# Kernel optimization log

Measured on AMD Instinct MI355X. Metric: run time of the kernel, lower is better.

The kernel has to match this reference:

```python
import jax, jax.numpy as jnp
import numpy as np

D_MODEL = 1024
HEADS = 16
D_K = D_MODEL // HEADS
B, S = 2, 2048
NEG = -1000000000.0

def setup_inputs() -> dict:
    key = jax.random.key(0)
    ks = jax.random.split(key, 11)
    sc = 1.0 / np.sqrt(D_MODEL)
    inp = {
        'q': jax.random.normal(ks[0], (B, S, D_MODEL), jnp.float32),
        'k': jax.random.normal(ks[1], (B, S, D_MODEL), jnp.float32),
        'v': jax.random.normal(ks[2], (B, S, D_MODEL), jnp.float32),
        'mask': jnp.tril(jnp.ones((S, S), jnp.int32))[None, None],  # causal [1,1,S,S]
        'wq_w': jax.random.normal(ks[3], (D_MODEL, D_MODEL), jnp.float32) * sc,
        'wq_b': jax.random.normal(ks[4], (D_MODEL,), jnp.float32) * 0.02,
        'wk_w': jax.random.normal(ks[5], (D_MODEL, D_MODEL), jnp.float32) * sc,
        'wk_b': jax.random.normal(ks[6], (D_MODEL,), jnp.float32) * 0.02,
        'wv_w': jax.random.normal(ks[7], (D_MODEL, D_MODEL), jnp.float32) * sc,
        'wv_b': jax.random.normal(ks[8], (D_MODEL,), jnp.float32) * 0.02,
        'wo_w': jax.random.normal(ks[9], (D_MODEL, D_MODEL), jnp.float32) * sc,
        'wo_b': jax.random.normal(ks[10], (D_MODEL,), jnp.float32) * 0.02,
    }
    return inp

def reference(q, k, v, mask, wq_w, wq_b, wk_w, wk_b, wv_w, wv_b, wo_w, wo_b):
    b, s, _ = q.shape
    # projections (torch Linear: x @ W^T + b)
    Q = (q @ wq_w.T + wq_b).reshape(b, s, HEADS, D_K).transpose(0, 2, 1, 3)  # [B,H,S,Dk]
    K = (k @ wk_w.T + wk_b).reshape(b, s, HEADS, D_K).transpose(0, 2, 1, 3)
    V = (v @ wv_w.T + wv_b).reshape(b, s, HEADS, D_K).transpose(0, 2, 1, 3)
    scores = jnp.einsum('bhqd,bhkd->bhqk', Q, K) / jnp.sqrt(jnp.float32(D_K))
    scores = jnp.where(mask == 0, NEG, scores)
    p = jax.nn.softmax(scores, axis=-1)  # dropout=0.0 -> identity
    x = jnp.einsum('bhqk,bhkd->bhqd', p, V)
    x = x.transpose(0, 2, 1, 3).reshape(b, s, D_MODEL)
    return x @ wo_w.T + wo_b
```

## Files before the change

kernel.cpp:

```cpp
#include <hip/hip_runtime.h>

typedef unsigned short u16;
typedef __attribute__((ext_vector_type(8))) short bf16x8;
typedef __attribute__((ext_vector_type(4))) float f32x4;

#define SEQ 2048
#define DMODEL 1024

__device__ __forceinline__ u16 f2bf(float f) {
    union { float f; unsigned u; } x; x.f = f;
    unsigned r = x.u + 0x7fffu + ((x.u >> 16) & 1u);
    return (u16)(r >> 16);
}

__device__ __forceinline__ u16 f2bf_trunc(float f) {
    union { float f; unsigned u; } x; x.f = f;
    return (u16)(x.u >> 16);
}

__device__ __forceinline__ float bf2f(u16 v) {
    union { unsigned u; float f; } x; x.u = ((unsigned)v) << 16;
    return x.f;
}

__device__ __forceinline__ f32x4 mfma16(bf16x8 a, bf16x8 b, f32x4 c) {
    return __builtin_amdgcn_mfma_f32_16x16x32_bf16(a, b, c, 0, 0, 0);
}

__device__ __forceinline__ void gld16(const u16* g, u16* l) {
    __builtin_amdgcn_global_load_lds(
        (__attribute__((address_space(1))) const void*)g,
        (__attribute__((address_space(3))) void*)l, 16, 0, 0);
}

struct CvtArgs {
    const float* src[7];
    u16* dst[7];
    int n4[7];
};

__global__ __launch_bounds__(256) void cvt_kernel(CvtArgs a) {
    const int id = blockIdx.y;
    const int i = blockIdx.x * 256 + threadIdx.x;
    if (i >= a.n4[id]) return;
    float4 f = ((const float4*)a.src[id])[i];
    ushort4 u;
    u.x = f2bf(f.x); u.y = f2bf(f.y); u.z = f2bf(f.z); u.w = f2bf(f.w);
    ((ushort4*)a.dst[id])[i] = u;
}


__global__ __launch_bounds__(512, 2) void gemm_qkv(
    const u16* __restrict__ Xq, const u16* __restrict__ Xk, const u16* __restrict__ Xv,
    const u16* __restrict__ Wq, const u16* __restrict__ Wk, const u16* __restrict__ Wv,
    const float* __restrict__ bq, const float* __restrict__ bk, const float* __restrict__ bv,
    u16* __restrict__ Qb, u16* __restrict__ Kb, u16* __restrict__ Vb)
{
    __shared__ u16 Abuf[2][256 * 64];
    __shared__ u16 Bbuf[2][256 * 64];

    const int bid = blockIdx.x;
    const int G = (bid & 7) * 24 + (bid >> 3);
    const int z = G >> 6;
    const int rem = G & 63;
    const int bm = (rem >> 2) * 256;
    const int bn = (rem & 3) * 256;

    const u16* X = (z == 0) ? Xq : (z == 1) ? Xk : Xv;
    const u16* W = (z == 0) ? Wq : (z == 1) ? Wk : Wv;
    const float* bias = (z == 0) ? bq : (z == 1) ? bk : bv;

    const int tid = threadIdx.x;
    const int lane = tid & 63, w = tid >> 6;
    const int wr = w >> 2, wc = w & 3;
    const int r = lane & 15, qd = lane >> 4;

    const int srow = lane >> 3;
    const int scol = ((lane & 7) ^ srow) * 8;
    const u16* Xs = X + (size_t)(bm + w * 32 + srow) * 1024 + scol;
    const u16* Ws = W + (size_t)(bn + w * 32 + srow) * 1024 + scol;

    const int rxor = (r & 7) << 4;
    const int rowA = (wr * 128 + r) * 128;
    const int rowB = (wc * 64 + r) * 128;
    const int ko0 = (qd * 16) ^ rxor;
    const int ko1 = (64 + qd * 16) ^ rxor;

    f32x4 acc[8][4];
    #pragma unroll
    for (int i = 0; i < 8; ++i)
        #pragma unroll
        for (int j = 0; j < 4; ++j)
            acc[i][j] = (f32x4){0.f, 0.f, 0.f, 0.f};

    auto stage = [&](int t) {
        const int d = t & 1;
        const u16* xa = Xs + t * 64;
        const u16* wb = Ws + t * 64;
        u16* Al = &Abuf[d][w * 2048];
        u16* Bl = &Bbuf[d][w * 2048];
        #pragma unroll
        for (int q = 0; q < 4; ++q) {
            gld16(xa + (size_t)q * 8192, Al + q * 512);
            gld16(wb + (size_t)q * 8192, Bl + q * 512);
        }
    };

    stage(0);
    stage(1);
    asm volatile("s_waitcnt vmcnt(8)" ::: "memory");
    __builtin_amdgcn_sched_barrier(0);
    __builtin_amdgcn_s_barrier();

    for (int t = 0; t < 16; ++t) {
        const u16* Ab = Abuf[t & 1];
        const u16* Bb = Bbuf[t & 1];
        #pragma unroll
        for (int kc = 0; kc < 2; ++kc) {
            const int ko = kc ? ko1 : ko0;
            bf16x8 aF[8], bF[4];
            #pragma unroll
            for (int m = 0; m < 8; ++m)
                aF[m] = *(const bf16x8*)((const char*)Ab + rowA + m * 2048 + ko);
            #pragma unroll
            for (int n = 0; n < 4; ++n)
                bF[n] = *(const bf16x8*)((const char*)Bb + rowB + n * 2048 + ko);
            __builtin_amdgcn_s_setprio(1);
            #pragma unroll
            for (int m = 0; m < 8; ++m)
                #pragma unroll
                for (int n = 0; n < 4; ++n)
                    acc[m][n] = mfma16(aF[m], bF[n], acc[m][n]);
            __builtin_amdgcn_s_setprio(0);
        }
        if (t == 15) break;
        asm volatile("s_waitcnt lgkmcnt(0)" ::: "memory");
        __builtin_amdgcn_sched_barrier(0);
        __builtin_amdgcn_s_barrier();
        if (t < 14) {
            stage(t + 2);
            asm volatile("s_waitcnt vmcnt(8)" ::: "memory");
        } else {
            asm volatile("s_waitcnt vmcnt(0)" ::: "memory");
        }
        __builtin_amdgcn_sched_barrier(0);
        __builtin_amdgcn_s_barrier();
        __builtin_amdgcn_sched_barrier(0);
    }

    const float scale = (z == 0) ? 0.125f : 1.0f;
    #pragma unroll
    for (int j = 0; j < 4; ++j) {
        const int n = bn + wc * 64 + j * 16 + r;
        const float bvl = bias[n];
        const int h = n >> 6, d = n & 63;
        #pragma unroll
        for (int i = 0; i < 8; ++i) {
            const int m0 = bm + wr * 128 + i * 16 + qd * 4;
            const int b_ = m0 >> 11, s0 = m0 & 2047;
            if (z == 0) {
                #pragma unroll
                for (int reg = 0; reg < 4; ++reg)
                    Qb[(size_t)(m0 + reg) * 1024 + n] = f2bf((acc[i][j][reg] + bvl) * scale);
            } else if (z == 1) {
                #pragma unroll
                for (int reg = 0; reg < 4; ++reg)
                    Kb[((size_t)(b_ * 16 + h) * SEQ + s0 + reg) * 64 + d] =
                        f2bf(acc[i][j][reg] + bvl);
            } else {
                ushort4 u;
                u.x = f2bf(acc[i][j][0] + bvl);
                u.y = f2bf(acc[i][j][1] + bvl);
                u.z = f2bf(acc[i][j][2] + bvl);
                u.w = f2bf(acc[i][j][3] + bvl);
                *(ushort4*)(Vb + ((size_t)(b_ * 16 + h) * 64 + d) * SEQ + s0) = u;
            }
        }
    }
}

__global__ __launch_bounds__(128, 3) void attn_kernel(
    const u16* __restrict__ Qb, const u16* __restrict__ Kb,
    const u16* __restrict__ Vb, u16* __restrict__ Op, float* __restrict__ Lp)
{
    __shared__ u16 Kst[2][4096];
    __shared__ u16 Vst[2][4096];
    __shared__ u16 Pst[2][16 * 72];

    const int bid = blockIdx.x;
    const int xcd = bid & 7;
    const int i2 = bid >> 3;
    const int bh = xcd + 8 * (i2 & 3);
    const int rest = i2 >> 2;
    const int g = 31 - (rest >> 1);
    const int half = rest & 1;
    const int b_ = bh >> 4, h = bh & 15;

    const int h0 = (g + 1) >> 1;
    const int j0 = half ? h0 : 0;
    const int j1 = half ? (g + 1) : h0;

    const int tid = threadIdx.x;
    const int lane = tid & 63, w = tid >> 6;
    const int r = lane & 15, qd = lane >> 4;

    const u16* Kh = Kb + (size_t)bh * SEQ * 64;
    const u16* Vh = Vb + (size_t)bh * 64 * SEQ;
    u16* Pw = Pst[w];

    bf16x8 aQ[2][2];
    #pragma unroll
    for (int i = 0; i < 2; ++i) {
        const size_t qoff =
            (size_t)(b_ * SEQ + g * 64 + w * 32 + i * 16 + r) * DMODEL + h * 64;
        aQ[i][0] = *(const bf16x8*)(Qb + qoff + qd * 8);
        aQ[i][1] = *(const bf16x8*)(Qb + qoff + 32 + qd * 8);
    }

    bf16x8 ones;
    #pragma unroll
    for (int e = 0; e < 8; ++e) ones[e] = (short)0x3F80;

    f32x4 o[2][4];
    f32x4 l[2];
    #pragma unroll
    for (int i = 0; i < 2; ++i) {
        l[i] = (f32x4){0.f, 0.f, 0.f, 0.f};
        #pragma unroll
        for (int db = 0; db < 4; ++db) o[i][db] = (f32x4){0.f, 0.f, 0.f, 0.f};
    }

    auto stage = [&](int j, int buf) {
        if (w == 0) {
            const u16* Kt = Kh + (size_t)j * 64 * 64;
            #pragma unroll
            for (int s = 0; s < 8; ++s)
                gld16(Kt + ((s >> 1) * 16 + r) * 64 + (s & 1) * 32 + qd * 8,
                      &Kst[buf][s * 512]);
        } else {
            const u16* Vt = Vh + j * 64;
            #pragma unroll
            for (int s = 0; s < 8; ++s)
                gld16(Vt + (size_t)((s >> 1) * 16 + r) * SEQ + (s & 1) * 32 + qd * 8,
                      &Vst[buf][s * 512]);
        }
    };

    if (j0 < j1) stage(j0, j0 & 1);

    for (int j = j0; j < j1; ++j) {
        const int cur = j & 1;
        __syncthreads();
        if (j + 1 < j1) stage(j + 1, 1 - cur);

        bf16x8 kf[4][2], vf[4][2];
        #pragma unroll
        for (int nb = 0; nb < 4; ++nb) {
            kf[nb][0] = *(const bf16x8*)(&Kst[cur][(nb * 2 + 0) * 512 + lane * 8]);
            kf[nb][1] = *(const bf16x8*)(&Kst[cur][(nb * 2 + 1) * 512 + lane * 8]);
        }
        #pragma unroll
        for (int db = 0; db < 4; ++db) {
            vf[db][0] = *(const bf16x8*)(&Vst[cur][(db * 2 + 0) * 512 + lane * 8]);
            vf[db][1] = *(const bf16x8*)(&Vst[cur][(db * 2 + 1) * 512 + lane * 8]);
        }

        #pragma unroll
        for (int i = 0; i < 2; ++i) {
            f32x4 sc[4];
            #pragma unroll
            for (int nb = 0; nb < 4; ++nb) {
                f32x4 s = (f32x4){0.f, 0.f, 0.f, 0.f};
                s = mfma16(kf[nb][0], aQ[i][0], s);
                s = mfma16(kf[nb][1], aQ[i][1], s);
                sc[nb] = s;
            }

            if (j == g) {
                const int rowr = w * 32 + i * 16 + r;
                #pragma unroll
                for (int nb = 0; nb < 4; ++nb)
                    #pragma unroll
                    for (int reg = 0; reg < 4; ++reg)
                        if (nb * 16 + qd * 4 + reg > rowr) sc[nb][reg] = -1e30f;
            }

            #pragma unroll
            for (int nb = 0; nb < 4; ++nb)
                #pragma unroll
                for (int reg = 0; reg < 4; ++reg)
                    sc[nb][reg] = exp2f(fmaf(sc[nb][reg], 1.4426950408889634f,
                                             -23.083120654223414f));

            #pragma unroll
            for (int nb = 0; nb < 4; ++nb) {
                ushort4 pk;
                pk.x = f2bf_trunc(sc[nb][0]);
                pk.y = f2bf_trunc(sc[nb][1]);
                pk.z = f2bf_trunc(sc[nb][2]);
                pk.w = f2bf_trunc(sc[nb][3]);
                *(ushort4*)(Pw + r * 72 + nb * 16 + qd * 4) = pk;
            }

            const bf16x8 aP0 = *(const bf16x8*)(Pw + r * 72 + qd * 8);
            const bf16x8 aP1 = *(const bf16x8*)(Pw + r * 72 + 32 + qd * 8);

            l[i] = mfma16(aP0, ones, l[i]);
            l[i] = mfma16(aP1, ones, l[i]);

            #pragma unroll
            for (int db = 0; db < 4; ++db) {
                o[i][db] = mfma16(aP0, vf[db][0], o[i][db]);
                o[i][db] = mfma16(aP1, vf[db][1], o[i][db]);
            }
        }
    }

    u16* Oh = Op + ((size_t)(half * 1024 + bh * 32 + g) * 4096);
    float* Lh = Lp + (size_t)(half * 1024 + bh * 32 + g) * 64;
    #pragma unroll
    for (int i = 0; i < 2; ++i) {
        #pragma unroll
        for (int db = 0; db < 4; ++db)
            #pragma unroll
            for (int reg = 0; reg < 4; ++reg)
                Oh[(w * 32 + i * 16 + qd * 4 + reg) * 64 + db * 16 + r] =
                    f2bf(o[i][db][reg]);
        if (r == 0) {
            #pragma unroll
            for (int reg = 0; reg < 4; ++reg)
                Lh[w * 32 + i * 16 + qd * 4 + reg] = l[i][reg];
        }
    }
}

__global__ __launch_bounds__(256) void attn_norm(
    const u16* __restrict__ Op, const float* __restrict__ Lp,
    u16* __restrict__ AO)
{
    const int idx = blockIdx.x * 256 + threadIdx.x;
    const int col8 = idx & 127;
    const int row = idx >> 7;
    const int h = col8 >> 3;
    const int b_ = row >> 11, s = row & 2047;
    const int g = s >> 6, r64 = s & 63;
    const int bh = b_ * 16 + h;

    const size_t pa = ((size_t)(bh * 32 + g) * 4096) + r64 * 64 + (col8 & 7) * 8;
    const size_t pb = pa + (size_t)1024 * 4096;
    const float la = Lp[(bh * 32 + g) * 64 + r64];
    const float lb = Lp[(1024 + bh * 32 + g) * 64 + r64];
    const float inv = 1.0f / (la + lb);

    const bf16x8 a = *(const bf16x8*)(Op + pa);
    const bf16x8 b = *(const bf16x8*)(Op + pb);
    bf16x8 o;
    #pragma unroll
    for (int e = 0; e < 8; ++e)
        o[e] = (short)f2bf((bf2f((u16)a[e]) + bf2f((u16)b[e])) * inv);
    *(bf16x8*)(AO + (size_t)row * 1024 + col8 * 8) = o;
}

__global__ __launch_bounds__(512, 2) void gemm_out(
    const u16* __restrict__ AO, const u16* __restrict__ W,
    const float* __restrict__ bias, float* __restrict__ out)
{
    __shared__ u16 Abuf[2][256 * 64];
    __shared__ u16 Bbuf[2][256 * 64];

    const int bid = blockIdx.x;
    const int G = (bid & 7) * 8 + (bid >> 3);
    const int bm = (G >> 2) * 256;
    const int bn = (G & 3) * 256;

    const int tid = threadIdx.x;
    const int lane = tid & 63, w = tid >> 6;
    const int wr = w >> 2, wc = w & 3;
    const int r = lane & 15, qd = lane >> 4;

    const int srow = lane >> 3;
    const int scol = ((lane & 7) ^ srow) * 8;
    const u16* Xs = AO + (size_t)(bm + w * 32 + srow) * 1024 + scol;
    const u16* Ws = W + (size_t)(bn + w * 32 + srow) * 1024 + scol;

    const int rxor = (r & 7) << 4;
    const int rowA = (wr * 128 + r) * 128;
    const int rowB = (wc * 64 + r) * 128;
    const int ko0 = (qd * 16) ^ rxor;
    const int ko1 = (64 + qd * 16) ^ rxor;

    f32x4 acc[8][4];
    #pragma unroll
    for (int i = 0; i < 8; ++i)
        #pragma unroll
        for (int j = 0; j < 4; ++j)
            acc[i][j] = (f32x4){0.f, 0.f, 0.f, 0.f};

    auto stage = [&](int t) {
        const int d = t & 1;
        const u16* xa = Xs + t * 64;
        const u16* wb = Ws + t * 64;
        u16* Al = &Abuf[d][w * 2048];
        u16* Bl = &Bbuf[d][w * 2048];
        #pragma unroll
        for (int q = 0; q < 4; ++q) {
            gld16(xa + (size_t)q * 8192, Al + q * 512);
            gld16(wb + (size_t)q * 8192, Bl + q * 512);
        }
    };

    stage(0);
    stage(1);
    asm volatile("s_waitcnt vmcnt(8)" ::: "memory");
    __builtin_amdgcn_sched_barrier(0);
    __builtin_amdgcn_s_barrier();

    for (int t = 0; t < 16; ++t) {
        const u16* Ab = Abuf[t & 1];
        const u16* Bb = Bbuf[t & 1];
        #pragma unroll
        for (int kc = 0; kc < 2; ++kc) {
            const int ko = kc ? ko1 : ko0;
            bf16x8 aF[8], bF[4];
            #pragma unroll
            for (int m = 0; m < 8; ++m)
                aF[m] = *(const bf16x8*)((const char*)Ab + rowA + m * 2048 + ko);
            #pragma unroll
            for (int n = 0; n < 4; ++n)
                bF[n] = *(const bf16x8*)((const char*)Bb + rowB + n * 2048 + ko);
            __builtin_amdgcn_s_setprio(1);
            #pragma unroll
            for (int m = 0; m < 8; ++m)
                #pragma unroll
                for (int n = 0; n < 4; ++n)
                    acc[m][n] = mfma16(aF[m], bF[n], acc[m][n]);
            __builtin_amdgcn_s_setprio(0);
        }
        if (t == 15) break;
        asm volatile("s_waitcnt lgkmcnt(0)" ::: "memory");
        __builtin_amdgcn_sched_barrier(0);
        __builtin_amdgcn_s_barrier();
        if (t < 14) {
            stage(t + 2);
            asm volatile("s_waitcnt vmcnt(8)" ::: "memory");
        } else {
            asm volatile("s_waitcnt vmcnt(0)" ::: "memory");
        }
        __builtin_amdgcn_sched_barrier(0);
        __builtin_amdgcn_s_barrier();
        __builtin_amdgcn_sched_barrier(0);
    }

    #pragma unroll
    for (int j = 0; j < 4; ++j) {
        const int n = bn + wc * 64 + j * 16 + r;
        const float bvl = bias[n];
        #pragma unroll
        for (int i = 0; i < 8; ++i) {
            const int m0 = bm + wr * 128 + i * 16 + qd * 4;
            #pragma unroll
            for (int reg = 0; reg < 4; ++reg)
                out[(size_t)(m0 + reg) * 1024 + n] = acc[i][j][reg] + bvl;
        }
    }
}

extern "C" void kernel_launch(void* const* d_in, const int* in_sizes, int n_in,
                              void* d_out, int out_size, void* d_ws, size_t ws_size,
                              hipStream_t stream) {
    const float* q  = (const float*)d_in[0];
    const float* k  = (const float*)d_in[1];
    const float* v  = (const float*)d_in[2];
    const float* wq = (const float*)d_in[4];
    const float* bq = (const float*)d_in[5];
    const float* wk = (const float*)d_in[6];
    const float* bk = (const float*)d_in[7];
    const float* wv = (const float*)d_in[8];
    const float* bv = (const float*)d_in[9];
    const float* wo = (const float*)d_in[10];
    const float* bo = (const float*)d_in[11];
    float* out = (float*)d_out;

    u16* ws = (u16*)d_ws;
    u16* Xq = ws;
    u16* Xk = Xq + (size_t)4194304;
    u16* Xv = Xk + (size_t)4194304;
    u16* Wq = Xv + (size_t)4194304;
    u16* Wk = Wq + (size_t)1048576;
    u16* Wv = Wk + (size_t)1048576;
    u16* Wo = Wv + (size_t)1048576;
    u16* Qb = Wo + (size_t)1048576;
    u16* Kb = Qb + (size_t)4194304;
    u16* Vb = Kb + (size_t)4194304;
    u16* AO = Vb + (size_t)4194304;

    u16* Op = ws;
    float* Lp = (float*)(ws + (size_t)8388608);

    CvtArgs ca;
    ca.src[0] = q;  ca.dst[0] = Xq; ca.n4[0] = 1048576;
    ca.src[1] = k;  ca.dst[1] = Xk; ca.n4[1] = 1048576;
    ca.src[2] = v;  ca.dst[2] = Xv; ca.n4[2] = 1048576;
    ca.src[3] = wq; ca.dst[3] = Wq; ca.n4[3] = 262144;
    ca.src[4] = wk; ca.dst[4] = Wk; ca.n4[4] = 262144;
    ca.src[5] = wv; ca.dst[5] = Wv; ca.n4[5] = 262144;
    ca.src[6] = wo; ca.dst[6] = Wo; ca.n4[6] = 262144;

    cvt_kernel<<<dim3(4096, 7), 256, 0, stream>>>(ca);
    gemm_qkv<<<dim3(192), 512, 0, stream>>>(Xq, Xk, Xv, Wq, Wk, Wv,
                                            bq, bk, bv, Qb, Kb, Vb);
    attn_kernel<<<dim3(2048), 128, 0, stream>>>(Qb, Kb, Vb, Op, Lp);
    attn_norm<<<dim3(2048), 256, 0, stream>>>(Op, Lp, AO);
    gemm_out<<<dim3(256 / 4), 512, 0, stream>>>(AO, Wo, bo, out);
}
```

Baseline: 258.3 us.

## Split causal attention KV range into thirds with four waves per block

The attention kernel now splits each query tile's causal KV range three ways instead of two, and uses four waves of 16 query rows each instead of two waves of 32 rows. The grid grows from 2048 to 3072 blocks of 256 threads. The normalisation kernel merges three partial outputs and three partial sums, and the Lp workspace offset moves to make room for the third partial. The aim is more parallelism and smaller per-thread register state for better occupancy, at the cost of one more partial write and read and less K/V reuse per block.

```diff
diff --git a/kernel.cpp b/kernel.cpp
--- a/kernel.cpp
+++ b/kernel.cpp
@@ -179,26 +179,27 @@
     }
 }
 
-__global__ __launch_bounds__(128, 3) void attn_kernel(
+__global__ __launch_bounds__(256, 3) void attn_kernel(
     const u16* __restrict__ Qb, const u16* __restrict__ Kb,
     const u16* __restrict__ Vb, u16* __restrict__ Op, float* __restrict__ Lp)
 {
     __shared__ u16 Kst[2][4096];
     __shared__ u16 Vst[2][4096];
-    __shared__ u16 Pst[2][16 * 72];
+    __shared__ u16 Pst[4][16 * 72];
 
     const int bid = blockIdx.x;
     const int xcd = bid & 7;
     const int i2 = bid >> 3;
     const int bh = xcd + 8 * (i2 & 3);
     const int rest = i2 >> 2;
-    const int g = 31 - (rest >> 1);
-    const int half = rest & 1;
+    const int gidx = rest / 3;
+    const int third = rest - gidx * 3;
+    const int g = 31 - gidx;
     const int b_ = bh >> 4, h = bh & 15;
 
-    const int h0 = (g + 1) >> 1;
-    const int j0 = half ? h0 : 0;
-    const int j1 = half ? (g + 1) : h0;
+    const int n = g + 1;
+    const int j0 = (n * third) / 3;
+    const int j1 = (n * (third + 1)) / 3;
 
     const int tid = threadIdx.x;
     const int lane = tid & 63, w = tid >> 6;
@@ -208,41 +209,40 @@
     const u16* Vh = Vb + (size_t)bh * 64 * SEQ;
     u16* Pw = Pst[w];
 
-    bf16x8 aQ[2][2];
-    #pragma unroll
-    for (int i = 0; i < 2; ++i) {
+    bf16x8 aQ[2];
+    {
         const size_t qoff =
-            (size_t)(b_ * SEQ + g * 64 + w * 32 + i * 16 + r) * DMODEL + h * 64;
-        aQ[i][0] = *(const bf16x8*)(Qb + qoff + qd * 8);
-        aQ[i][1] = *(const bf16x8*)(Qb + qoff + 32 + qd * 8);
+            (size_t)(b_ * SEQ + g * 64 + w * 16 + r) * DMODEL + h * 64;
+        aQ[0] = *(const bf16x8*)(Qb + qoff + qd * 8);
+        aQ[1] = *(const bf16x8*)(Qb + qoff + 32 + qd * 8);
     }
 
     bf16x8 ones;
     #pragma unroll
     for (int e = 0; e < 8; ++e) ones[e] = (short)0x3F80;
 
-    f32x4 o[2][4];
-    f32x4 l[2];
-    #pragma unroll
-    for (int i = 0; i < 2; ++i) {
-        l[i] = (f32x4){0.f, 0.f, 0.f, 0.f};
-        #pragma unroll
-        for (int db = 0; db < 4; ++db) o[i][db] = (f32x4){0.f, 0.f, 0.f, 0.f};
-    }
+    f32x4 o[4];
+    f32x4 l = (f32x4){0.f, 0.f, 0.f, 0.f};
+    #pragma unroll
+    for (int db = 0; db < 4; ++db) o[db] = (f32x4){0.f, 0.f, 0.f, 0.f};
 
     auto stage = [&](int j, int buf) {
-        if (w == 0) {
+        if (w < 2) {
             const u16* Kt = Kh + (size_t)j * 64 * 64;
             #pragma unroll
-            for (int s = 0; s < 8; ++s)
-                gld16(Kt + ((s >> 1) * 16 + r) * 64 + (s & 1) * 32 + qd * 8,
-                      &Kst[buf][s * 512]);
+            for (int s = 0; s < 4; ++s) {
+                const int ss = w * 4 + s;
+                gld16(Kt + ((ss >> 1) * 16 + r) * 64 + (ss & 1) * 32 + qd * 8,
+                      &Kst[buf][ss * 512]);
+            }
         } else {
             const u16* Vt = Vh + j * 64;
             #pragma unroll
-            for (int s = 0; s < 8; ++s)
-                gld16(Vt + (size_t)((s >> 1) * 16 + r) * SEQ + (s & 1) * 32 + qd * 8,
-                      &Vst[buf][s * 512]);
+            for (int s = 0; s < 4; ++s) {
+                const int ss = (w - 2) * 4 + s;
+                gld16(Vt + (size_t)((ss >> 1) * 16 + r) * SEQ + (ss & 1) * 32 + qd * 8,
+                      &Vst[buf][ss * 512]);
+            }
         }
     };
 
@@ -265,72 +265,65 @@
             vf[db][1] = *(const bf16x8*)(&Vst[cur][(db * 2 + 1) * 512 + lane * 8]);
         }
 
-        #pragma unroll
-        for (int i = 0; i < 2; ++i) {
-            f32x4 sc[4];
-            #pragma unroll
-            for (int nb = 0; nb < 4; ++nb) {
-                f32x4 s = (f32x4){0.f, 0.f, 0.f, 0.f};
-                s = mfma16(kf[nb][0], aQ[i][0], s);
-                s = mfma16(kf[nb][1], aQ[i][1], s);
-                sc[nb] = s;
-            }
-
-            if (j == g) {
-                const int rowr = w * 32 + i * 16 + r;
-                #pragma unroll
-                for (int nb = 0; nb < 4; ++nb)
-                    #pragma unroll
-                    for (int reg = 0; reg < 4; ++reg)
-                        if (nb * 16 + qd * 4 + reg > rowr) sc[nb][reg] = -1e30f;
-            }
-
+        f32x4 sc[4];
+        #pragma unroll
+        for (int nb = 0; nb < 4; ++nb) {
+            f32x4 s = (f32x4){0.f, 0.f, 0.f, 0.f};
+            s = mfma16(kf[nb][0], aQ[0], s);
+            s = mfma16(kf[nb][1], aQ[1], s);
+            sc[nb] = s;
+        }
+
+        if (j == g) {
+            const int rowr = w * 16 + r;
             #pragma unroll
             for (int nb = 0; nb < 4; ++nb)
                 #pragma unroll
                 for (int reg = 0; reg < 4; ++reg)
-                    sc[nb][reg] = exp2f(fmaf(sc[nb][reg], 1.4426950408889634f,
-                                             -23.083120654223414f));
-
-            #pragma unroll
-            for (int nb = 0; nb < 4; ++nb) {
-                ushort4 pk;
-                pk.x = f2bf_trunc(sc[nb][0]);
-                pk.y = f2bf_trunc(sc[nb][1]);
-                pk.z = f2bf_trunc(sc[nb][2]);
-                pk.w = f2bf_trunc(sc[nb][3]);
-                *(ushort4*)(Pw + r * 72 + nb * 16 + qd * 4) = pk;
-            }
-
-            const bf16x8 aP0 = *(const bf16x8*)(Pw + r * 72 + qd * 8);
-            const bf16x8 aP1 = *(const bf16x8*)(Pw + r * 72 + 32 + qd * 8);
-
-            l[i] = mfma16(aP0, ones, l[i]);
-            l[i] = mfma16(aP1, ones, l[i]);
-
-            #pragma unroll
-            for (int db = 0; db < 4; ++db) {
-                o[i][db] = mfma16(aP0, vf[db][0], o[i][db]);
-                o[i][db] = mfma16(aP1, vf[db][1], o[i][db]);
-            }
-        }
-    }
-
-    u16* Oh = Op + ((size_t)(half * 1024 + bh * 32 + g) * 4096);
-    float* Lh = Lp + (size_t)(half * 1024 + bh * 32 + g) * 64;
-    #pragma unroll
-    for (int i = 0; i < 2; ++i) {
-        #pragma unroll
-        for (int db = 0; db < 4; ++db)
+                    if (nb * 16 + qd * 4 + reg > rowr) sc[nb][reg] = -1e30f;
+        }
+
+        #pragma unroll
+        for (int nb = 0; nb < 4; ++nb)
             #pragma unroll
             for (int reg = 0; reg < 4; ++reg)
-                Oh[(w * 32 + i * 16 + qd * 4 + reg) * 64 + db * 16 + r] =
-                    f2bf(o[i][db][reg]);
-        if (r == 0) {
-            #pragma unroll
-            for (int reg = 0; reg < 4; ++reg)
-                Lh[w * 32 + i * 16 + qd * 4 + reg] = l[i][reg];
-        }
+                sc[nb][reg] = exp2f(fmaf(sc[nb][reg], 1.4426950408889634f,
+                                         -23.083120654223414f));
+
+        #pragma unroll
+        for (int nb = 0; nb < 4; ++nb) {
+            ushort4 pk;
+            pk.x = f2bf_trunc(sc[nb][0]);
+            pk.y = f2bf_trunc(sc[nb][1]);
+            pk.z = f2bf_trunc(sc[nb][2]);
+            pk.w = f2bf_trunc(sc[nb][3]);
+            *(ushort4*)(Pw + r * 72 + nb * 16 + qd * 4) = pk;
+        }
+
+        const bf16x8 aP0 = *(const bf16x8*)(Pw + r * 72 + qd * 8);
+        const bf16x8 aP1 = *(const bf16x8*)(Pw + r * 72 + 32 + qd * 8);
+
+        l = mfma16(aP0, ones, l);
+        l = mfma16(aP1, ones, l);
+
+        #pragma unroll
+        for (int db = 0; db < 4; ++db) {
+            o[db] = mfma16(aP0, vf[db][0], o[db]);
+            o[db] = mfma16(aP1, vf[db][1], o[db]);
+        }
+    }
+
+    u16* Oh = Op + ((size_t)(third * 1024 + bh * 32 + g) * 4096);
+    float* Lh = Lp + (size_t)(third * 1024 + bh * 32 + g) * 64;
+    #pragma unroll
+    for (int db = 0; db < 4; ++db)
+        #pragma unroll
+        for (int reg = 0; reg < 4; ++reg)
+            Oh[(w * 16 + qd * 4 + reg) * 64 + db * 16 + r] = f2bf(o[db][reg]);
+    if (r == 0) {
+        #pragma unroll
+        for (int reg = 0; reg < 4; ++reg)
+            Lh[w * 16 + qd * 4 + reg] = l[reg];
     }
 }
 
@@ -348,16 +341,19 @@
 
     const size_t pa = ((size_t)(bh * 32 + g) * 4096) + r64 * 64 + (col8 & 7) * 8;
     const size_t pb = pa + (size_t)1024 * 4096;
+    const size_t pc = pb + (size_t)1024 * 4096;
     const float la = Lp[(bh * 32 + g) * 64 + r64];
     const float lb = Lp[(1024 + bh * 32 + g) * 64 + r64];
-    const float inv = 1.0f / (la + lb);
+    const float lc = Lp[(2048 + bh * 32 + g) * 64 + r64];
+    const float inv = 1.0f / (la + lb + lc);
 
     const bf16x8 a = *(const bf16x8*)(Op + pa);
     const bf16x8 b = *(const bf16x8*)(Op + pb);
+    const bf16x8 c = *(const bf16x8*)(Op + pc);
     bf16x8 o;
     #pragma unroll
     for (int e = 0; e < 8; ++e)
-        o[e] = (short)f2bf((bf2f((u16)a[e]) + bf2f((u16)b[e])) * inv);
+        o[e] = (short)f2bf((bf2f((u16)a[e]) + bf2f((u16)b[e]) + bf2f((u16)c[e])) * inv);
     *(bf16x8*)(AO + (size_t)row * 1024 + col8 * 8) = o;
 }
 
@@ -495,7 +491,7 @@
     u16* AO = Vb + (size_t)4194304;
 
     u16* Op = ws;
-    float* Lp = (float*)(ws + (size_t)8388608);
+    float* Lp = (float*)(ws + (size_t)12582912);
 
     CvtArgs ca;
     ca.src[0] = q;  ca.dst[0] = Xq; ca.n4[0] = 1048576;
@@ -509,7 +505,7 @@
     cvt_kernel<<<dim3(4096, 7), 256, 0, stream>>>(ca);
     gemm_qkv<<<dim3(192), 512, 0, stream>>>(Xq, Xk, Xv, Wq, Wk, Wv,
                                             bq, bk, bv, Qb, Kb, Vb);
-    attn_kernel<<<dim3(2048), 128, 0, stream>>>(Qb, Kb, Vb, Op, Lp);
+    attn_kernel<<<dim3(3072), 256, 0, stream>>>(Qb, Kb, Vb, Op, Lp);
     attn_norm<<<dim3(2048), 256, 0, stream>>>(Op, Lp, AO);
-    gemm_out<<<dim3(256 / 4), 512, 0, stream>>>(AO, Wo, bo, out);
-}
+    gemm_out<<<dim3(64), 512, 0, stream>>>(AO, Wo, bo, out);
+}
```

Measured after the change: 256.4 us. Within noise of the previous version (-0.8%).
